# Performance work log

Hardware: AMD Instinct MI355X
Metric: run time of the kernel (lower is better)

The kernel has to match this reference:

```python
import jax, jax.numpy as jnp
import numpy as np
from jax import lax


def setup_inputs() -> dict:
    key = jax.random.key(0)
    k1, k2, k3 = jax.random.split(key, 3)
    N, C, H, W = 16, 256, 128, 128
    KH = KW = 3
    x = jax.random.normal(k1, (N, C, H, W), dtype=jnp.float32)
    # kaiming-uniform-ish scale for a 3x3 depthwise kernel (fan_in = 9)
    weight = jax.random.normal(k2, (C, 1, KH, KW), dtype=jnp.float32) * (1.0 / 3.0)
    bias = jax.random.normal(k3, (C,), dtype=jnp.float32) * 0.01
    return {"x": x, "weight": weight, "bias": bias}


def reference(x, weight, bias):
    # Depthwise conv2d: groups == in_channels, stride=1, padding=1.
    # weight: (C, 1, KH, KW) in torch OIHW layout with feature_group_count=C.
    C = x.shape[1]
    y = lax.conv_general_dilated(
        x, weight,
        window_strides=(1, 1),
        padding=((1, 1), (1, 1)),
        dimension_numbers=("NCHW", "OIHW", "NCHW"),
        feature_group_count=C,
    )
    y = y + bias[None, :, None, None]
    return y.astype(jnp.float32)
```

## Files before the change

### kernel.cpp

```cpp
#include <hip/hip_runtime.h>


constexpr int N_ = 16;
constexpr int C_ = 256;
constexpr int H_ = 128;
constexpr int W_ = 128;
constexpr int ROWS_PER_BLOCK = 8;
constexpr int TILES_PER_PLANE = H_ / ROWS_PER_BLOCK;

__global__ __launch_bounds__(256) void dwconv3x3_kernel(
    const float* __restrict__ x,
    const float* __restrict__ weight,
    const float* __restrict__ bias,
    float* __restrict__ out) {

    const int lane = threadIdx.x & 31;
    const int ty   = threadIdx.x >> 5;

    const int bid  = blockIdx.x;
    const int tile = bid & (TILES_PER_PLANE - 1);
    const int nc   = bid >> 4;
    const int c    = nc & (C_ - 1);

    const int h  = tile * ROWS_PER_BLOCK + ty;
    const int w0 = lane * 4;

    const float* __restrict__ xp = x + (size_t)nc * (H_ * W_);
    float* __restrict__ op = out + (size_t)nc * (H_ * W_) + h * W_ + w0;

    const float* wp = weight + c * 9;
    const float w00 = wp[0], w01 = wp[1], w02 = wp[2];
    const float w10 = wp[3], w11 = wp[4], w12 = wp[5];
    const float w20 = wp[6], w21 = wp[7], w22 = wp[8];
    const float b = bias[c];

    float e[3][6];
#pragma unroll
    for (int kr = 0; kr < 3; ++kr) {
        const int r = h + kr - 1;
        if (r < 0 || r >= H_) {
#pragma unroll
            for (int j = 0; j < 6; ++j) e[kr][j] = 0.0f;
        } else {
            const float4 v = *(const float4*)(xp + r * W_ + w0);
            e[kr][1] = v.x; e[kr][2] = v.y; e[kr][3] = v.z; e[kr][4] = v.w;
            e[kr][0] = (w0 > 0)       ? xp[r * W_ + w0 - 1] : 0.0f;
            e[kr][5] = (w0 + 4 < W_)  ? xp[r * W_ + w0 + 4] : 0.0f;
        }
    }

    float o[4];
#pragma unroll
    for (int j = 0; j < 4; ++j) {
        float s = b;
        s = fmaf(w00, e[0][j],     s);
        s = fmaf(w01, e[0][j + 1], s);
        s = fmaf(w02, e[0][j + 2], s);
        s = fmaf(w10, e[1][j],     s);
        s = fmaf(w11, e[1][j + 1], s);
        s = fmaf(w12, e[1][j + 2], s);
        s = fmaf(w20, e[2][j],     s);
        s = fmaf(w21, e[2][j + 1], s);
        s = fmaf(w22, e[2][j + 2], s);
        o[j] = s;
    }

    float4 ov;
    ov.x = o[0]; ov.y = o[1]; ov.z = o[2]; ov.w = o[3];
    *(float4*)op = ov;
}

extern "C" void kernel_launch(void* const* d_in, const int* in_sizes, int n_in,
                              void* d_out, int out_size, void* d_ws, size_t ws_size,
                              hipStream_t stream) {
    const float* x      = (const float*)d_in[0];
    const float* weight = (const float*)d_in[1];
    const float* bias   = (const float*)d_in[2];
    float* out          = (float*)d_out;

    const int grid = N_ * C_ * TILES_PER_PLANE;
    dwconv3x3_kernel<<<grid, 256, 0, stream>>>(x, weight, bias, out);
}
```

Before: 491.7 us.

## Register-block four output rows per thread and use shuffles for halo columns

```diff
diff --git a/kernel.cpp b/kernel.cpp
--- a/kernel.cpp
+++ b/kernel.cpp
@@ -5,7 +5,9 @@
 constexpr int C_ = 256;
 constexpr int H_ = 128;
 constexpr int W_ = 128;
-constexpr int ROWS_PER_BLOCK = 8;
+constexpr int ROWS_PER_THREAD = 4;
+constexpr int TY_PER_BLOCK = 8;
+constexpr int ROWS_PER_BLOCK = ROWS_PER_THREAD * TY_PER_BLOCK;
 constexpr int TILES_PER_PLANE = H_ / ROWS_PER_BLOCK;
 
 __global__ __launch_bounds__(256) void dwconv3x3_kernel(
@@ -19,55 +21,71 @@
 
     const int bid  = blockIdx.x;
     const int tile = bid & (TILES_PER_PLANE - 1);
-    const int nc   = bid >> 4;
+    const int nc   = bid >> 2;
     const int c    = nc & (C_ - 1);
 
-    const int h  = tile * ROWS_PER_BLOCK + ty;
+    const int h0 = tile * ROWS_PER_BLOCK + ty * ROWS_PER_THREAD;
     const int w0 = lane * 4;
 
     const float* __restrict__ xp = x + (size_t)nc * (H_ * W_);
-    float* __restrict__ op = out + (size_t)nc * (H_ * W_) + h * W_ + w0;
+    float* __restrict__ op = out + (size_t)nc * (H_ * W_);
 
     const float* wp = weight + c * 9;
-    const float w00 = wp[0], w01 = wp[1], w02 = wp[2];
-    const float w10 = wp[3], w11 = wp[4], w12 = wp[5];
-    const float w20 = wp[6], w21 = wp[7], w22 = wp[8];
+    float wgt[3][3];
+#pragma unroll
+    for (int k = 0; k < 3; ++k) {
+#pragma unroll
+        for (int j = 0; j < 3; ++j) wgt[k][j] = wp[k * 3 + j];
+    }
     const float b = bias[c];
 
-    float e[3][6];
+    float4 rows[6];
 #pragma unroll
-    for (int kr = 0; kr < 3; ++kr) {
-        const int r = h + kr - 1;
-        if (r < 0 || r >= H_) {
-#pragma unroll
-            for (int j = 0; j < 6; ++j) e[kr][j] = 0.0f;
+    for (int i = 0; i < 6; ++i) {
+        const int r = h0 - 1 + i;
+        if (r >= 0 && r < H_) {
+            rows[i] = *(const float4*)(xp + r * W_ + w0);
         } else {
-            const float4 v = *(const float4*)(xp + r * W_ + w0);
-            e[kr][1] = v.x; e[kr][2] = v.y; e[kr][3] = v.z; e[kr][4] = v.w;
-            e[kr][0] = (w0 > 0)       ? xp[r * W_ + w0 - 1] : 0.0f;
-            e[kr][5] = (w0 + 4 < W_)  ? xp[r * W_ + w0 + 4] : 0.0f;
+            rows[i] = make_float4(0.f, 0.f, 0.f, 0.f);
         }
     }
 
-    float o[4];
+    float acc[ROWS_PER_THREAD][4];
 #pragma unroll
-    for (int j = 0; j < 4; ++j) {
-        float s = b;
-        s = fmaf(w00, e[0][j],     s);
-        s = fmaf(w01, e[0][j + 1], s);
-        s = fmaf(w02, e[0][j + 2], s);
-        s = fmaf(w10, e[1][j],     s);
-        s = fmaf(w11, e[1][j + 1], s);
-        s = fmaf(w12, e[1][j + 2], s);
-        s = fmaf(w20, e[2][j],     s);
-        s = fmaf(w21, e[2][j + 1], s);
-        s = fmaf(w22, e[2][j + 2], s);
-        o[j] = s;
+    for (int o = 0; o < ROWS_PER_THREAD; ++o)
+#pragma unroll
+        for (int j = 0; j < 4; ++j) acc[o][j] = b;
+
+#pragma unroll
+    for (int i = 0; i < 6; ++i) {
+        float e0 = __shfl_up(rows[i].w, 1, 32);
+        if (lane == 0) e0 = 0.f;
+        float e5 = __shfl_down(rows[i].x, 1, 32);
+        if (lane == 31) e5 = 0.f;
+        const float e[6] = {e0, rows[i].x, rows[i].y, rows[i].z, rows[i].w, e5};
+
+        const int olo = (i >= 2) ? (i - 2) : 0;
+        const int ohi = (i < ROWS_PER_THREAD) ? i : (ROWS_PER_THREAD - 1);
+#pragma unroll
+        for (int o = olo; o <= ohi; ++o) {
+            const int k = i - o;
+#pragma unroll
+            for (int j = 0; j < 4; ++j) {
+                float s = acc[o][j];
+                s = fmaf(wgt[k][0], e[j],     s);
+                s = fmaf(wgt[k][1], e[j + 1], s);
+                s = fmaf(wgt[k][2], e[j + 2], s);
+                acc[o][j] = s;
+            }
+        }
     }
 
-    float4 ov;
-    ov.x = o[0]; ov.y = o[1]; ov.z = o[2]; ov.w = o[3];
-    *(float4*)op = ov;
+#pragma unroll
+    for (int o = 0; o < ROWS_PER_THREAD; ++o) {
+        float4 ov;
+        ov.x = acc[o][0]; ov.y = acc[o][1]; ov.z = acc[o][2]; ov.w = acc[o][3];
+        *(float4*)(op + (h0 + o) * W_ + w0) = ov;
+    }
 }
 
 extern "C" void kernel_launch(void* const* d_in, const int* in_sizes, int n_in,
```

Result: faster. 433.0 us (-11.9%).
